# Kernel optimization log

Measured on AMD Instinct MI355X. Metric: run time of the kernel, lower is better.

## Reference

```python
import jax, jax.numpy as jnp
from jax import lax
import numpy as np

B, L, D = 2048, 100, 64      # batch, max_len, embedding_dim
K = 64                       # embedding_num (codebook entries)
CB = K * 8                   # code_book_dim = 512 (== D*8 encoder out channels)
ITEMS = 1_000_000
EPS = 1e-3                   # tf.layers.batch_normalization default epsilon


def setup_inputs() -> dict:
    key = jax.random.key(0)
    ks = jax.random.split(key, 16)
    w = lambda i, shape: jax.random.normal(ks[i], shape, dtype=jnp.float32) * 0.05
    z = lambda c: jnp.zeros((c,), jnp.float32)
    o = lambda c: jnp.ones((c,), jnp.float32)
    return {
        "history_item_ids": jax.random.randint(ks[0], (B, L), 0, ITEMS, dtype=jnp.int32),
        "history_item_masks": jax.random.randint(ks[1], (B, L), 0, 2, dtype=jnp.int32),
        "item_embedding_table": jax.random.normal(ks[2], (ITEMS, D), dtype=jnp.float32),
        "user_book": jax.random.normal(ks[3], (K, CB), dtype=jnp.float32),
        "e_w1": w(4, (2, 2, D, 2 * D)), "e_b1": z(2 * D), "e_g1": o(2 * D), "e_be1": z(2 * D),
        "e_w2": w(5, (2, 2, 2 * D, 4 * D)), "e_b2": z(4 * D), "e_g2": o(4 * D), "e_be2": z(4 * D),
        "e_w3": w(6, (2, 2, 4 * D, 8 * D)), "e_b3": z(8 * D),
        "d_w1": w(7, (2, 2, 8 * D, 4 * D)), "d_b1": z(4 * D), "d_g1": o(4 * D), "d_be1": z(4 * D),
        "d_w2": w(8, (2, 2, 4 * D, 2 * D)), "d_b2": z(2 * D), "d_g2": o(2 * D), "d_be2": z(2 * D),
        "d_w3": w(9, (2, 2, 2 * D, D)), "d_b3": z(D),
    }


def _forward(history_item_ids, history_item_masks, item_embedding_table, user_book,
             e_w1, e_b1, e_g1, e_be1, e_w2, e_b2, e_g2, e_be2, e_w3, e_b3,
             d_w1, d_b1, d_g1, d_be1, d_w2, d_b2, d_g2, d_be2, d_w3, d_b3):
    dn = ('NHWC', 'HWIO', 'NHWC')
    bn = lambda x, g, b: x * (g / jnp.sqrt(1.0 + EPS)) + b  # inference BN: moving mean 0, var 1
    conv = lambda x, w_, b_: lax.conv_general_dilated(x, w_, (1, 1), 'VALID', dimension_numbers=dn) + b_
    deconv = lambda x, w_, b_: lax.conv_transpose(x, w_, (1, 1), 'VALID', dimension_numbers=dn) + b_

    mask = (history_item_masks >= 1).astype(jnp.float32)               # [B,L]
    hist = item_embedding_table[history_item_ids] * mask[..., None]    # [B,L,D]

    H = int(L ** 0.5); W = L // H
    h = hist.reshape(-1, H, W, D)
    h = jax.nn.relu(bn(conv(h, e_w1, e_b1), e_g1, e_be1))              # [B,9,9,2D]
    h = jax.nn.relu(bn(conv(h, e_w2, e_b2), e_g2, e_be2))              # [B,8,8,4D]
    x_encode = conv(h, e_w3, e_b3)                                     # [B,7,7,CB]

    # nearest-neighbor codebook lookup (get_quantized)
    flat = x_encode.reshape(-1, CB)                                    # [B*49,CB]
    dist = ((flat * flat).sum(1, keepdims=True)
            + (user_book * user_book).sum(1)
            - 2.0 * flat @ user_book.T)                                # [B*49,K]
    idx = jnp.argmin(dist, axis=1)
    quantized = user_book[idx].reshape(x_encode.shape)                 # [B,7,7,CB]

    # straight-through estimator
    st = x_encode + lax.stop_gradient(quantized - x_encode)
    g = jax.nn.relu(bn(deconv(st, d_w1, d_b1), d_g1, d_be1))           # [B,8,8,4D]
    g = jax.nn.relu(bn(deconv(g, d_w2, d_b2), d_g2, d_be2))            # [B,9,9,2D]
    vq_x = deconv(g, d_w3, d_b3).reshape(hist.shape)                   # [B,L,D]

    vq_mean = vq_x.sum(1) / mask.sum(-1, keepdims=True)                # [B,D]
    mse = lambda a, b: jnp.mean((a - b) ** 2)
    beta = 0.25
    vqvae_loss = (mse(hist, vq_x)
                  + mse(quantized, lax.stop_gradient(x_encode))
                  + beta * mse(x_encode, lax.stop_gradient(quantized)))
    return vq_mean, vq_x, vqvae_loss


def reference(history_item_ids, history_item_masks, item_embedding_table, user_book,
              e_w1, e_b1, e_g1, e_be1, e_w2, e_b2, e_g2, e_be2, e_w3, e_b3,
              d_w1, d_b1, d_g1, d_be1, d_w2, d_b2, d_g2, d_be2, d_w3, d_b3):
    return _forward(history_item_ids, history_item_masks, item_embedding_table, user_book,
                    e_w1, e_b1, e_g1, e_be1, e_w2, e_b2, e_g2, e_be2, e_w3, e_b3,
                    d_w1, d_b1, d_g1, d_be1, d_w2, d_b2, d_g2, d_be2, d_w3, d_b3)
```

## Files before the change

kernel.cpp:

```cpp
#include <hip/hip_runtime.h>
#include <hip/hip_bf16.h>
#include <cstdint>
#include <cstddef>


typedef __attribute__((ext_vector_type(8))) short short8v;
typedef __attribute__((ext_vector_type(4))) float f32x4;

constexpr int B  = 2048;
constexpr int L  = 100;
constexpr int K  = 64;
constexpr int CB = 512;
#define MARGIN 0.1f

constexpr size_t R0_OFF  = 0;
constexpr size_t R1_OFF  = 51380224;
constexpr size_t IDX_OFF = 84934656;
constexpr size_t CBN_OFF = 85035008;
constexpr size_t CNT_OFF = 85035072;
constexpr size_t ACC_OFF = 85035088;
constexpr size_t WL_OFF  = 85035104;
constexpr size_t WB_OFF  = 85135456;

constexpr size_t EW1H=0,       EW1L=32768;
constexpr size_t EW2H=65536,   EW2L=196608;
constexpr size_t EW3H=327680;
constexpr size_t DW2H=851968,  DW3H=983040;
constexpr size_t W3BH=1015808, W3BL=1081344;

constexpr size_t BW1_OFF  = WB_OFF + 573440;
constexpr size_t DOTB_OFF = BW1_OFF + 65536;

__device__ inline ushort bf16_hi(float f){ __hip_bfloat16 h=__float2bfloat16(f); return *(ushort*)&h; }
__device__ inline float  bf16_tof(ushort u){ __hip_bfloat16 h; *(ushort*)&h=u; return __bfloat162float(h); }

__device__ void wtrans(const float* __restrict__ w, int IC, int OC,
                       ushort* __restrict__ hi, ushort* __restrict__ lo,
                       int gid, int gsz)
{
    int tot = 4*IC*OC;
    for (int i = gid; i < tot; i += gsz) {
        int kk = i/(IC*OC), r = i - kk*(IC*OC), ic = r/OC, oc = r - ic*OC;
        float v = w[i];
        ushort h = bf16_hi(v);
        size_t dst = ((size_t)kk*OC + oc)*IC + ic;
        hi[dst] = h;
        if (lo) lo[dst] = bf16_hi(v - bf16_tof(h));
    }
}

__global__ __launch_bounds__(256)
void wprep_k(const float* e1, const float* e2, const float* e3,
             const float* d2, const float* d3, ushort* wb)
{
    int gid = blockIdx.x*256 + threadIdx.x, gsz = gridDim.x*256;
    wtrans(e1,  64, 128, wb+EW1H, wb+EW1L, gid, gsz);
    wtrans(e2, 128, 256, wb+EW2H, wb+EW2L, gid, gsz);
    wtrans(e3, 256, 512, wb+EW3H, nullptr, gid, gsz);
    wtrans(d2, 256, 128, wb+DW2H, nullptr, gid, gsz);
    wtrans(d3, 128,  64, wb+DW3H, nullptr, gid, gsz);
}

__global__ __launch_bounds__(256)
void w3b_k(const float* __restrict__ e_w3, const float* __restrict__ book,
           ushort* __restrict__ wb)
{
    const int kk = blockIdx.x >> 6, k = blockIdx.x & 63, ic = threadIdx.x;
    const float4* wr = (const float4*)(e_w3 + ((size_t)(kk*256)+ic)*512);
    const float4* br = (const float4*)(book + (size_t)k*512);
    float s = 0.f;
    for (int c = 0; c < 128; ++c) {
        float4 a = wr[c], bb = br[c];
        s = fmaf(a.x,bb.x,fmaf(a.y,bb.y,fmaf(a.z,bb.z,fmaf(a.w,bb.w,s))));
    }
    size_t dst = ((size_t)(kk*64+k))*256 + ic;
    ushort h = bf16_hi(s);
    wb[W3BH+dst] = h;
    wb[W3BL+dst] = bf16_hi(s - bf16_tof(h));
}

__global__ __launch_bounds__(256)
void bw1_k(const float* __restrict__ d_w1, const float* __restrict__ book,
           float* __restrict__ bw1)
{
    const int tap = blockIdx.x >> 6, k = blockIdx.x & 63, oc = threadIdx.x;
    const float* br = book + (size_t)k*512;
    const float* wr = d_w1 + (size_t)(tap*512)*256 + oc;
    float s = 0.f;
    for (int ic = 0; ic < 512; ++ic)
        s = fmaf(br[ic], wr[(size_t)ic*256], s);
    bw1[((size_t)(tap*64+k))*256 + oc] = s;
}

__global__ __launch_bounds__(256)
void prep_k(const float* __restrict__ book, const float* __restrict__ e_b3,
            float* __restrict__ cbn, float* __restrict__ dotb,
            float* __restrict__ acc, int* __restrict__ cnt)
{
    const int t = threadIdx.x;
    if (t < 64) {
        const float* r = book + t * 512;
        float s = 0.f, d = 0.f;
        for (int c = 0; c < 512; ++c) { s = fmaf(r[c], r[c], s); d = fmaf(e_b3[c], r[c], d); }
        cbn[t] = s; dotb[t] = d;
    }
    if (t == 64 || t == 65) acc[t-64] = 0.f;
    if (t == 66) *cnt = 0;
}

template<int IH,int IW,int IC,int OC,int PAD,int MODE,bool HASBN,bool SPLIT,
         int OCS,int ICC,int MT,int OUTFMT,bool FUSE,int SMP,bool DBUF>
__global__ __launch_bounds__(256)
void sconv_k(const uint* __restrict__ in_pk, const ushort* __restrict__ in_bf,
             const int* __restrict__ ids, const int* __restrict__ masks,
             const float* __restrict__ table,
             const ushort* __restrict__ wt_hi, const ushort* __restrict__ wt_lo,
             const float* __restrict__ bias, const float* __restrict__ gamma,
             const float* __restrict__ beta,
             float* __restrict__ out_f, uint* __restrict__ out_pk,
             ushort* __restrict__ out_bf, float* __restrict__ out_mean,
             float* __restrict__ acc_g)
{
    constexpr int OH=IH+2*PAD-1, OW=IW+2*PAD-1, NPOS=OH*OW, IHW=IH*IW;
    constexpr int OCB=OC/OCS, NPW=OCB/4, NT=NPW/16;
    constexpr int NCH=IC/ICC, KS=ICC/32;
    constexpr int PL=SPLIT?2:1;
    constexpr int NB=(DBUF && NCH>1)?2:1;
    constexpr int AROWS=IHW+1, RB=ICC*2;
    constexpr int C8=ICC/8;
    constexpr int NITEMS=SMP*IHW*C8;
    constexpr int SI=(NITEMS+255)/256;
    constexpr bool EXACT=(SI*256==NITEMS);
    constexpr int SPLB=AROWS*RB;
    constexpr int SAMB=PL*SPLB;
    constexpr int BUFB=SMP*SAMB;

    __shared__ ushort s_a[NB*SMP*PL*AROWS*ICC];
    char* sb=(char*)s_a;

    const int v=blockIdx.x, r8=v&7, iv=v>>3;
    const int b0 = (r8*(B/SMP/8) + iv/OCS)*SMP;
    const int sl = iv - (iv/OCS)*OCS;

    const int tid=threadIdx.x, lane=tid&63, wv=tid>>6;
    const int l15=lane&15, lq=lane>>4;
    const int n0=sl*OCB + wv*NPW;

    int arow[4][MT];
    #pragma unroll
    for(int kk=0;kk<4;++kk){
        const int ky=kk>>1, kx=kk&1;
        #pragma unroll
        for(int m=0;m<MT;++m){
            int p=m*16+l15;
            int py=p/OW, px=p-py*OW;
            int ty=py+ky-PAD, tx=px+kx-PAD;
            bool ok=(p<NPOS)&&((unsigned)ty<(unsigned)IH)&&((unsigned)tx<(unsigned)IW);
            arow[kk][m]= ok ? ty*IW+tx : IHW;
        }
    }

    f32x4 acc[SMP][MT][NT];
    #pragma unroll
    for(int s=0;s<SMP;++s)
        #pragma unroll
        for(int m=0;m<MT;++m)
            #pragma unroll
            for(int n=0;n<NT;++n) acc[s][m][n]=(f32x4)0.0f;

    uint4 r0[SI];
    uint4 r1[(MODE==1||MODE==3)?SI:1];
    float msk[(MODE==1)?SI:1];

    auto stage_load=[&](int c){
        const int ic0=c*ICC;
        #pragma unroll
        for(int t=0;t<SI;++t){
            int idx=tid+t*256;
            if(EXACT || idx<NITEMS){
                int row=idx/C8, g=idx-row*C8;
                int s=row/IHW, r=row-s*IHW;
                if constexpr(MODE==1){
                    int id=ids[(b0+s)*L+r];
                    msk[t]=(masks[(b0+s)*L+r]>=1)?1.f:0.f;
                    const float* src=table+(size_t)id*64+g*8;
                    r0[t]=*(const uint4*)src;
                    r1[t]=*(const uint4*)(src+4);
                } else if constexpr(MODE==3){
                    const uint* src=in_pk+((size_t)(b0+s)*IHW+r)*IC+ic0+g*8;
                    r0[t]=*(const uint4*)src;
                    r1[t]=*(const uint4*)(src+4);
                } else {
                    r0[t]=*(const uint4*)(in_bf+((size_t)(b0+s)*IHW+r)*IC+ic0+g*8);
                }
            }
        }
    };

    auto stage_write=[&](int bufb){
        #pragma unroll
        for(int t=0;t<SI;++t){
            int idx=tid+t*256;
            if(EXACT || idx<NITEMS){
                int row=idx/C8, g=idx-row*C8;
                int s=row/IHW, r=row-s*IHW;
                int boff=bufb + s*SAMB + r*RB + ((g^(r&7))<<4);
                if constexpr(MODE==1){
                    const float* f0=(const float*)&r0[t];
                    const float* f1=(const float*)&r1[t];
                    float vv[8]={f0[0]*msk[t],f0[1]*msk[t],f0[2]*msk[t],f0[3]*msk[t],
                                 f1[0]*msk[t],f1[1]*msk[t],f1[2]*msk[t],f1[3]*msk[t]};
                    ushort hh[8], ll[8];
                    #pragma unroll
                    for(int j=0;j<8;++j){ hh[j]=bf16_hi(vv[j]); ll[j]=bf16_hi(vv[j]-bf16_tof(hh[j])); }
                    *(uint4*)(sb+boff)=*(uint4*)hh;
                    *(uint4*)(sb+SPLB+boff)=*(uint4*)ll;
                } else if constexpr(MODE==3){
                    const uint* u0=(const uint*)&r0[t];
                    const uint* u1=(const uint*)&r1[t];
                    ushort hh[8], ll[8];
                    #pragma unroll
                    for(int j=0;j<4;++j){ hh[j]=(ushort)(u0[j]&0xffffu); ll[j]=(ushort)(u0[j]>>16); }
                    #pragma unroll
                    for(int j=0;j<4;++j){ hh[4+j]=(ushort)(u1[j]&0xffffu); ll[4+j]=(ushort)(u1[j]>>16); }
                    *(uint4*)(sb+boff)=*(uint4*)hh;
                    *(uint4*)(sb+SPLB+boff)=*(uint4*)ll;
                } else {
                    *(uint4*)(sb+boff)=r0[t];
                }
            }
        }
    };

    auto zero_rows=[&](){
        for(int z=tid; z<NB*SMP*PL*C8; z+=256){
            int nb=z/(SMP*PL*C8), rz=z-nb*(SMP*PL*C8);
            int s=rz/(PL*C8), rz2=rz-s*(PL*C8), pl=rz2/C8, g=rz2-pl*C8;
            *(uint4*)(sb + nb*BUFB + s*SAMB + pl*SPLB + IHW*RB + (g<<4)) = make_uint4(0,0,0,0);
        }
    };

    auto do_mfma=[&](int bufb, int c){
        const int ic0=c*ICC;
        __builtin_amdgcn_s_setprio(1);
        #pragma unroll
        for(int kk=0;kk<4;++kk){
            #pragma unroll
            for(int ks=0;ks<KS;++ks){
                short8v bhv[NT]; short8v blv[SPLIT?NT:1];
                #pragma unroll
                for(int n=0;n<NT;++n){
                    int col=n0+n*16+l15;
                    size_t widx=((size_t)kk*OC+col)*IC+ic0+ks*32+lq*8;
                    bhv[n]=*(const short8v*)(wt_hi+widx);
                    if constexpr(SPLIT) blv[n]=*(const short8v*)(wt_lo+widx);
                }
                #pragma unroll
                for(int s=0;s<SMP;++s){
                    const int sbase=bufb + s*SAMB;
                    #pragma unroll
                    for(int m=0;m<MT;++m){
                        int off=sbase + arow[kk][m]*RB + ((((ks<<2)|lq)^(arow[kk][m]&7))<<4);
                        short8v ah=*(const short8v*)(sb+off);
                        if constexpr(SPLIT){
                            short8v al=*(const short8v*)(sb+SPLB+off);
                            #pragma unroll
                            for(int n=0;n<NT;++n){
                                acc[s][m][n]=__builtin_amdgcn_mfma_f32_16x16x32_bf16(ah,bhv[n],acc[s][m][n],0,0,0);
                                acc[s][m][n]=__builtin_amdgcn_mfma_f32_16x16x32_bf16(ah,blv[n],acc[s][m][n],0,0,0);
                                acc[s][m][n]=__builtin_amdgcn_mfma_f32_16x16x32_bf16(al,bhv[n],acc[s][m][n],0,0,0);
                            }
                        } else {
                            #pragma unroll
                            for(int n=0;n<NT;++n)
                                acc[s][m][n]=__builtin_amdgcn_mfma_f32_16x16x32_bf16(ah,bhv[n],acc[s][m][n],0,0,0);
                        }
                    }
                }
            }
        }
        __builtin_amdgcn_s_setprio(0);
    };

    if constexpr(NB==1){
        stage_load(0);
        zero_rows();
        for(int c=0;c<NCH;++c){
            if(c) __syncthreads();
            stage_write(0);
            __syncthreads();
            if(c+1<NCH) stage_load(c+1);
            do_mfma(0,c);
        }
    } else {
        stage_load(0);
        stage_write(0);
        zero_rows();
        __syncthreads();
        for(int c=0;c<NCH;++c){
            if(c+1<NCH) stage_load(c+1);
            do_mfma((c&1)*BUFB,c);
            if(c+1<NCH){
                stage_write(((c+1)&1)*BUFB);
                __syncthreads();
            }
        }
    }

    const float rs=(float)(1.0/sqrt(1.0+1e-3));
    float lsum=0.f, colsum=0.f;
    #pragma unroll
    for(int s=0;s<SMP;++s){
        const int b=b0+s;
        #pragma unroll
        for(int n=0;n<NT;++n){
            int col=n0+n*16+l15;
            float bi=bias[col];
            float gsc=0.f, bt=0.f;
            if constexpr(HASBN){ gsc=gamma[col]*rs; bt=beta[col]; }
            #pragma unroll
            for(int m=0;m<MT;++m){
                #pragma unroll
                for(int j=0;j<4;++j){
                    int p=m*16+lq*4+j;
                    if(p<NPOS){
                        float vx=acc[s][m][n][j]+bi;
                        if constexpr(HASBN) vx=fmaxf(fmaf(vx,gsc,bt),0.f);
                        size_t g=(size_t)b*NPOS+p;
                        if constexpr(OUTFMT==0){
                            out_f[g*OC+col]=vx;
                        } else if constexpr(OUTFMT==1){
                            ushort h=bf16_hi(vx);
                            ushort lo=bf16_hi(vx-bf16_tof(h));
                            out_pk[g*OC+col]=(uint)h | ((uint)lo<<16);
                        } else {
                            out_bf[g*OC+col]=bf16_hi(vx);
                        }
                        if constexpr(FUSE){
                            int id=ids[b*L+p];
                            float mm=(masks[b*L+p]>=1)?1.f:0.f;
                            float h=table[(size_t)id*64+col]*mm;
                            float df=h-vx;
                            lsum=fmaf(df,df,lsum);
                            colsum+=vx;
                        }
                    }
                }
            }
        }
    }

    if constexpr(FUSE){
        const int b=b0;
        float mc=0.f;
        for(int l=lane;l<L;l+=64) mc += (masks[b*L+l]>=1)?1.f:0.f;
        #pragma unroll
        for(int off=32;off;off>>=1) mc+=__shfl_xor(mc,off);
        colsum += __shfl_xor(colsum,16);
        colsum += __shfl_xor(colsum,32);
        if(lq==0) out_mean[b*64 + n0 + l15] = colsum/mc;
        #pragma unroll
        for(int off=32;off;off>>=1) lsum+=__shfl_xor(lsum,off);
        __syncthreads();
        float* red=(float*)sb;
        if(lane==0) red[wv]=lsum;
        __syncthreads();
        if(tid==0) atomicAdd(acc_g+0, red[0]+red[1]+red[2]+red[3]);
    }
}

__global__ __launch_bounds__(512)
void mxnd_k(const uint* __restrict__ in_pk,
            const ushort* __restrict__ wx,
            const ushort* __restrict__ w3bh, const ushort* __restrict__ w3bl,
            const float* __restrict__ xbias,
            const float* __restrict__ cbn, const float* __restrict__ dotb,
            int* __restrict__ qidx, float* __restrict__ acc_g,
            int* __restrict__ cnt, int* __restrict__ wl)
{
    constexpr int IHW=64, AROWS=65, RB=128;
    constexpr int NPOS=49, OW=7, MT=4, NT=4;
    constexpr int SPLB=AROWS*RB;
    constexpr int BUFB=2*SPLB;

    __shared__ ushort s_a[2*2*AROWS*64];
    char* sb=(char*)s_a;

    const int v=blockIdx.x;
    const int b=(v&7)*(B/8)+(v>>3);
    const int tid=threadIdx.x, lane=tid&63, wv=tid>>6;
    const int l15=lane&15, lq=lane>>4;
    const int n0x=wv*64;

    int arow[4][MT];
    #pragma unroll
    for(int kk=0;kk<4;++kk){
        const int ky=kk>>1, kx=kk&1;
        #pragma unroll
        for(int m=0;m<MT;++m){
            int p=m*16+l15;
            int py=p/OW, px=p-py*OW;
            arow[kk][m]= (p<NPOS) ? (py+ky)*8+(px+kx) : IHW;
        }
    }

    f32x4 accx[MT][NT];
    #pragma unroll
    for(int m=0;m<MT;++m)
        #pragma unroll
        for(int n=0;n<NT;++n) accx[m][n]=(f32x4)0.0f;
    f32x4 accd[MT];
    #pragma unroll
    for(int m=0;m<MT;++m) accd[m]=(f32x4)0.0f;

    uint4 r0, r1;

    auto stage_load=[&](int c){
        const int ic0=c*64;
        int row=tid>>3, g=tid&7;
        const uint* src=in_pk+((size_t)b*IHW+row)*256+ic0+g*8;
        r0=*(const uint4*)src;
        r1=*(const uint4*)(src+4);
    };
    auto stage_write=[&](int bufb){
        int row=tid>>3, g=tid&7;
        int boff=bufb + row*RB + ((g^(row&7))<<4);
        const uint* u0=(const uint*)&r0;
        const uint* u1=(const uint*)&r1;
        ushort hh[8], ll[8];
        #pragma unroll
        for(int j=0;j<4;++j){ hh[j]=(ushort)(u0[j]&0xffffu); ll[j]=(ushort)(u0[j]>>16); }
        #pragma unroll
        for(int j=0;j<4;++j){ hh[4+j]=(ushort)(u1[j]&0xffffu); ll[4+j]=(ushort)(u1[j]>>16); }
        *(uint4*)(sb+boff)=*(uint4*)hh;
        *(uint4*)(sb+SPLB+boff)=*(uint4*)ll;
    };

    stage_load(0);
    stage_write(0);
    for(int z=tid; z<2*2*8; z+=512){
        int nb=z/16, rz=z-nb*16, pl=rz/8, g=rz-pl*8;
        *(uint4*)(sb + nb*BUFB + pl*SPLB + IHW*RB + (g<<4)) = make_uint4(0,0,0,0);
    }
    __syncthreads();

    for(int c=0;c<4;++c){
        if(c+1<4) stage_load(c+1);
        const int bufb=(c&1)*BUFB;
        const int ic0=c*64;
        __builtin_amdgcn_s_setprio(1);
        #pragma unroll
        for(int kk=0;kk<4;++kk){
            #pragma unroll
            for(int ks=0;ks<2;++ks){
                short8v bx[NT];
                #pragma unroll
                for(int n=0;n<NT;++n){
                    int col=n0x+n*16+l15;
                    bx[n]=*(const short8v*)(wx+((size_t)kk*512+col)*256+ic0+ks*32+lq*8);
                }
                short8v bdh, bdl;
                if(wv<4){
                    int cold=wv*16+l15;
                    size_t wdx=((size_t)kk*64+cold)*256+ic0+ks*32+lq*8;
                    bdh=*(const short8v*)(w3bh+wdx);
                    bdl=*(const short8v*)(w3bl+wdx);
                }
                #pragma unroll
                for(int m=0;m<MT;++m){
                    int off=bufb + arow[kk][m]*RB + ((((ks<<2)|lq)^(arow[kk][m]&7))<<4);
                    short8v ah=*(const short8v*)(sb+off);
                    #pragma unroll
                    for(int n=0;n<NT;++n)
                        accx[m][n]=__builtin_amdgcn_mfma_f32_16x16x32_bf16(ah,bx[n],accx[m][n],0,0,0);
                    if(wv<4){
                        short8v al=*(const short8v*)(sb+SPLB+off);
                        accd[m]=__builtin_amdgcn_mfma_f32_16x16x32_bf16(ah,bdh,accd[m],0,0,0);
                        accd[m]=__builtin_amdgcn_mfma_f32_16x16x32_bf16(ah,bdl,accd[m],0,0,0);
                        accd[m]=__builtin_amdgcn_mfma_f32_16x16x32_bf16(al,bdh,accd[m],0,0,0);
                    }
                }
            }
        }
        __builtin_amdgcn_s_setprio(0);
        if(c+1<4){
            stage_write(((c+1)&1)*BUFB);
            __syncthreads();
        }
    }

    float xs=0.f;
    #pragma unroll
    for(int n=0;n<NT;++n){
        int col=n0x+n*16+l15;
        float bi=xbias[col];
        #pragma unroll
        for(int m=0;m<MT;++m){
            #pragma unroll
            for(int j=0;j<4;++j){
                int p=m*16+lq*4+j;
                if(p<NPOS){ float vv=accx[m][n][j]+bi; xs=fmaf(vv,vv,xs); }
            }
        }
    }
    #pragma unroll
    for(int off=32;off;off>>=1) xs+=__shfl_xor(xs,off);
    __syncthreads();
    float* f=(float*)sb;
    if(lane==0) f[wv]=xs;

    if(wv<4){
        float cb=cbn[wv*16+l15], db=dotb[wv*16+l15];
        float* sd1=f+16;
        int*   sk =(int*)(f+16+256);
        float* sd2=f+16+512;
        #pragma unroll
        for(int m=0;m<MT;++m){
            #pragma unroll
            for(int j=0;j<4;++j){
                int p=m*16+lq*4+j;
                float d1=cb-2.f*(accd[m][j]+db);
                int   k1=wv*16+l15;
                float d2=3.4e38f;
                #pragma unroll
                for(int off=1;off<16;off<<=1){
                    float od1=__shfl_xor(d1,off);
                    int   ok1=__shfl_xor(k1,off);
                    float od2=__shfl_xor(d2,off);
                    if(od1<d1 || (od1==d1 && ok1<k1)){ d2=fminf(d1,od2); d1=od1; k1=ok1; }
                    else                              { d2=fminf(d2,od1); }
                }
                if(l15==0 && p<NPOS){ sd1[p*4+wv]=d1; sk[p*4+wv]=k1; sd2[p*4+wv]=d2; }
            }
        }
    }
    __syncthreads();
    if(tid==0) atomicAdd(acc_g+1, f[0]+f[1]+f[2]+f[3]+f[4]+f[5]+f[6]+f[7]);

    {
        float* sd1=f+16;
        int*   sk =(int*)(f+16+256);
        float* sd2=f+16+512;
        float lsum=0.f;
        if(tid<NPOS){
            float d1=sd1[tid*4+0]; int k1=sk[tid*4+0]; float d2=sd2[tid*4+0];
            #pragma unroll
            for(int w=1;w<4;++w){
                float D1=sd1[tid*4+w]; int K1=sk[tid*4+w]; float D2=sd2[tid*4+w];
                if(D1<d1){ d2=fminf(d1,D2); d1=D1; k1=K1; }
                else     { d2=fminf(d2,D1); }
            }
            qidx[b*49+tid]=k1;
            if(d2-d1<=MARGIN){ int t=atomicAdd(cnt,1); wl[t]=b*49+tid; }
            lsum=d1;
        }
        if(tid<64){
            #pragma unroll
            for(int off=32;off;off>>=1) lsum+=__shfl_xor(lsum,off);
            if(tid==0) atomicAdd(acc_g+1, lsum);
        }
    }
}

__global__ __launch_bounds__(256)
void dgather_k(const int* __restrict__ qidx, const float* __restrict__ bw1,
               const float* __restrict__ b1, const float* __restrict__ g1s,
               const float* __restrict__ be1, ushort* __restrict__ G1)
{
    const int b=blockIdx.x, tid=threadIdx.x;
    const int pg=tid>>2, og=(tid&3)*64;
    const int py=pg>>3, px=pg&7;

    float a[64];
    #pragma unroll
    for(int j=0;j<64;++j) a[j]=0.f;

    #pragma unroll
    for(int tap=0;tap<4;++tap){
        int iy=py+(tap>>1)-1, ix=px+(tap&1)-1;
        if((unsigned)iy<7u && (unsigned)ix<7u){
            int kq=qidx[b*49+iy*7+ix];
            const float4* src=(const float4*)(bw1+((size_t)(tap*64+kq))*256+og);
            #pragma unroll
            for(int j=0;j<16;++j){
                float4 vv=src[j];
                a[4*j+0]+=vv.x; a[4*j+1]+=vv.y; a[4*j+2]+=vv.z; a[4*j+3]+=vv.w;
            }
        }
    }
    const float rs=(float)(1.0/sqrt(1.0+1e-3));
    #pragma unroll
    for(int j=0;j<64;++j){
        int col=og+j;
        float vv=a[j]+b1[col];
        vv=fmaxf(fmaf(vv, g1s[col]*rs, be1[col]), 0.f);
        G1[((size_t)b*64+pg)*256+col]=bf16_hi(vv);
    }
}

__global__ __launch_bounds__(256)
void recompute_k(const int* __restrict__ wl, const int* __restrict__ cnt,
                 const int* __restrict__ ids, const int* __restrict__ masks,
                 const float* __restrict__ table, const float* __restrict__ book,
                 const float* __restrict__ e_w1, const float* __restrict__ e_b1,
                 const float* __restrict__ e_g1, const float* __restrict__ e_be1,
                 const float* __restrict__ e_w2, const float* __restrict__ e_b2,
                 const float* __restrict__ e_g2, const float* __restrict__ e_be2,
                 const float* __restrict__ e_w3, const float* __restrict__ e_b3,
                 int* __restrict__ qidx)
{
    __shared__ double s_h[16*64];
    __shared__ double s_a1[9*128];
    __shared__ double s_a2[4*256];
    __shared__ double s_x[512];
    __shared__ double s_d[256];

    const int tid = threadIdx.x;
    const double rs = 1.0 / sqrt(1.0 + 1e-3);
    const int n = *cnt;

    for (int wi = blockIdx.x; wi < n; wi += gridDim.x) {
        const int row = wl[wi];
        const int b = row / 49, p = row % 49;
        const int py = p / 7, px = p % 7;

        for (int i = tid; i < 16*64; i += 256) {
            int cell = i >> 6, d = i & 63;
            int l = (py + (cell >> 2)) * 10 + (px + (cell & 3));
            int id = ids[b*100 + l];
            double m = (masks[b*100 + l] >= 1) ? 1.0 : 0.0;
            s_h[i] = (double)table[(size_t)id*64 + d] * m;
        }
        __syncthreads();

        for (int i = tid; i < 9*128; i += 256) {
            int cell = i >> 7, oc = i & 127;
            int ry = cell / 3, rx = cell % 3;
            double s = 0.0;
            #pragma unroll
            for (int kk = 0; kk < 4; ++kk) {
                int icell = (ry + (kk>>1))*4 + (rx + (kk&1));
                const double* hh = s_h + icell*64;
                const float* ww = e_w1 + (kk*64)*128 + oc;
                for (int ic = 0; ic < 64; ++ic)
                    s = fma(hh[ic], (double)ww[ic*128], s);
            }
            s += (double)e_b1[oc];
            s = s * ((double)e_g1[oc] * rs) + (double)e_be1[oc];
            s_a1[i] = s > 0.0 ? s : 0.0;
        }
        __syncthreads();

        for (int i = tid; i < 4*256; i += 256) {
            int cell = i >> 8, oc = i & 255;
            int qy = cell >> 1, qx = cell & 1;
            double s = 0.0;
            #pragma unroll
            for (int kk = 0; kk < 4; ++kk) {
                int icell = (qy + (kk>>1))*3 + (qx + (kk&1));
                const double* aa = s_a1 + icell*128;
                const float* ww = e_w2 + (kk*128)*256 + oc;
                for (int ic = 0; ic < 128; ++ic)
                    s = fma(aa[ic], (double)ww[ic*256], s);
            }
            s += (double)e_b2[oc];
            s = s * ((double)e_g2[oc] * rs) + (double)e_be2[oc];
            s_a2[i] = s > 0.0 ? s : 0.0;
        }
        __syncthreads();

        for (int i = tid; i < 512; i += 256) {
            double s = 0.0;
            #pragma unroll
            for (int kk = 0; kk < 4; ++kk) {
                const double* aa = s_a2 + kk*256;
                const float* ww = e_w3 + (kk*256)*512 + i;
                for (int ic = 0; ic < 256; ++ic)
                    s = fma(aa[ic], (double)ww[ic*512], s);
            }
            s_x[i] = s + (double)e_b3[i];
        }
        __syncthreads();

        {
            int k = tid & 63, seg = tid >> 6;
            const float* cr = book + k*512 + seg*128;
            const double* xr = s_x + seg*128;
            double s = 0.0;
            for (int c = 0; c < 128; ++c) {
                double dd = xr[c] - (double)cr[c];
                s = fma(dd, dd, s);
            }
            s_d[seg*64 + k] = s;
        }
        __syncthreads();

        if (tid < 64) {
            double dv = s_d[tid] + s_d[64+tid] + s_d[128+tid] + s_d[192+tid];
            int kk2 = tid;
            #pragma unroll
            for (int off = 32; off > 0; off >>= 1) {
                double od = __shfl_xor(dv, off);
                int    ok = __shfl_xor(kk2, off);
                if (od < dv || (od == dv && ok < kk2)) { dv = od; kk2 = ok; }
            }
            if (tid == 0) qidx[row] = kk2;
        }
        __syncthreads();
    }
}

__global__ void loss_k(const float* __restrict__ acc, float* __restrict__ out_loss)
{
    float l1 = acc[0] / 13107200.f;
    float l2 = acc[1] / 51380224.f;
    out_loss[0] = l1 + l2 + 0.25f * l2;
}

extern "C" void kernel_launch(void* const* d_in, const int* in_sizes, int n_in,
                              void* d_out, int out_size, void* d_ws, size_t ws_size,
                              hipStream_t stream)
{
    const int*   ids   = (const int*)d_in[0];
    const int*   masks = (const int*)d_in[1];
    const float* table = (const float*)d_in[2];
    const float* book  = (const float*)d_in[3];
    const float* e_w1  = (const float*)d_in[4];
    const float* e_b1  = (const float*)d_in[5];
    const float* e_g1  = (const float*)d_in[6];
    const float* e_be1 = (const float*)d_in[7];
    const float* e_w2  = (const float*)d_in[8];
    const float* e_b2  = (const float*)d_in[9];
    const float* e_g2  = (const float*)d_in[10];
    const float* e_be2 = (const float*)d_in[11];
    const float* e_w3  = (const float*)d_in[12];
    const float* e_b3  = (const float*)d_in[13];
    const float* d_w1  = (const float*)d_in[14];
    const float* d_b1  = (const float*)d_in[15];
    const float* d_g1  = (const float*)d_in[16];
    const float* d_be1 = (const float*)d_in[17];
    const float* d_w2  = (const float*)d_in[18];
    const float* d_b2  = (const float*)d_in[19];
    const float* d_g2  = (const float*)d_in[20];
    const float* d_be2 = (const float*)d_in[21];
    const float* d_w3  = (const float*)d_in[22];
    const float* d_b3  = (const float*)d_in[23];

    float*  ws  = (float*)d_ws;
    uint*   A1P = (uint*)(ws + R0_OFF);
    uint*   A2P = (uint*)(ws + R1_OFF);
    ushort* G1  = (ushort*)(ws + R1_OFF);
    ushort* G2  = (ushort*)(ws + R0_OFF);
    int*    IDX = (int*)(ws + IDX_OFF);
    float*  CBN = ws + CBN_OFF;
    int*    CNT = (int*)(ws + CNT_OFF);
    float*  ACC = ws + ACC_OFF;
    int*    WL  = (int*)(ws + WL_OFF);
    ushort* WB  = (ushort*)(ws + WB_OFF);
    float*  BW1 = ws + BW1_OFF;
    float*  DOTB= ws + DOTB_OFF;

    float* out_mean = (float*)d_out;
    float* out_vqx  = (float*)d_out + (size_t)B * 64;
    float* out_loss = (float*)d_out + (size_t)B * 64 + (size_t)B * L * 64;

    prep_k<<<1, 256, 0, stream>>>(book, e_b3, CBN, DOTB, ACC, CNT);
    wprep_k<<<512, 256, 0, stream>>>(e_w1, e_w2, e_w3, d_w2, d_w3, WB);
    w3b_k<<<256, 256, 0, stream>>>(e_w3, book, WB);
    bw1_k<<<256, 256, 0, stream>>>(d_w1, book, BW1);

    sconv_k<10,10, 64,128,0,1,true ,true ,1, 64,6,1,false,1,true ><<<B,    256,0,stream>>>(
        nullptr, nullptr, ids, masks, table,
        WB+EW1H, WB+EW1L, e_b1, e_g1, e_be1, nullptr, A1P, nullptr, nullptr, nullptr);
    sconv_k< 9, 9,128,256,0,3,true ,true ,2, 64,4,1,false,2,false><<<B,    256,0,stream>>>(
        A1P, nullptr, nullptr, nullptr, nullptr,
        WB+EW2H, WB+EW2L, e_b2, e_g2, e_be2, nullptr, A2P, nullptr, nullptr, nullptr);

    mxnd_k<<<B, 512, 0, stream>>>(A2P, WB+EW3H, WB+W3BH, WB+W3BL,
                                  e_b3, CBN, DOTB, IDX, ACC, CNT, WL);

    recompute_k<<<512, 256, 0, stream>>>(WL, CNT, ids, masks, table, book,
                                         e_w1, e_b1, e_g1, e_be1,
                                         e_w2, e_b2, e_g2, e_be2,
                                         e_w3, e_b3, IDX);

    dgather_k<<<B, 256, 0, stream>>>(IDX, BW1, d_b1, d_g1, d_be1, G1);
    sconv_k< 8, 8,256,128,1,4,true ,false,1, 64,6,2,false,2,true ><<<B/2,  256,0,stream>>>(
        nullptr, G1, nullptr, nullptr, nullptr,
        WB+DW2H, nullptr, d_b2, d_g2, d_be2, nullptr, nullptr, G2, nullptr, nullptr);
    sconv_k< 9, 9,128, 64,1,4,false,false,1, 64,7,0,true ,1,true ><<<B,    256,0,stream>>>(
        nullptr, G2, ids, masks, table,
        WB+DW3H, nullptr, d_b3, nullptr, nullptr, out_vqx, nullptr, nullptr, out_mean, ACC);

    loss_k<<<1, 1, 0, stream>>>(ACC, out_loss);
}
```

Before: 1.310 ms.

## Stage full encoder-conv3 input in LDS once and retune conv grid splits

The encoder's third conv plus codebook distance kernel now loads the whole 64x256 packed input tile into shared memory once, with a 32-way XOR swizzle, instead of double-buffering four 64-channel chunks with a sync per chunk. It also drops the zero pad row and sets launch bounds to 4 blocks per CU. Two sconv launches change a template parameter, so encoder conv2 runs on twice as many blocks and decoder conv2 runs one batch item per block. This removes per-chunk barriers and adds parallelism, but the larger LDS footprint (64KB) may limit occupancy.

```diff
diff --git a/kernel.cpp b/kernel.cpp
--- a/kernel.cpp
+++ b/kernel.cpp
@@ -369,8 +369,8 @@
     }
 }
 
-__global__ __launch_bounds__(512)
-void mxnd_k(const uint* __restrict__ in_pk,
+__global__ __launch_bounds__(512,4)
+void xnd2_k(const uint* __restrict__ in_pk,
             const ushort* __restrict__ wx,
             const ushort* __restrict__ w3bh, const ushort* __restrict__ w3bl,
             const float* __restrict__ xbias,
@@ -378,12 +378,11 @@
             int* __restrict__ qidx, float* __restrict__ acc_g,
             int* __restrict__ cnt, int* __restrict__ wl)
 {
-    constexpr int IHW=64, AROWS=65, RB=128;
     constexpr int NPOS=49, OW=7, MT=4, NT=4;
-    constexpr int SPLB=AROWS*RB;
-    constexpr int BUFB=2*SPLB;
-
-    __shared__ ushort s_a[2*2*AROWS*64];
+    constexpr int ROWB=512;
+    constexpr int PLB=64*ROWB;
+
+    __shared__ ushort s_a[2*64*256];
     char* sb=(char*)s_a;
 
     const int v=blockIdx.x;
@@ -392,6 +391,25 @@
     const int l15=lane&15, lq=lane>>4;
     const int n0x=wv*64;
 
+    #pragma unroll
+    for(int t=0;t<4;++t){
+        int idx=tid+t*512;
+        int row=idx>>5, sl=idx&31;
+        const uint* src=in_pk+((size_t)b*64+row)*256+sl*8;
+        uint4 u0=*(const uint4*)src, u1=*(const uint4*)(src+4);
+        const uint* p0=(const uint*)&u0;
+        const uint* p1=(const uint*)&u1;
+        ushort hh[8], ll[8];
+        #pragma unroll
+        for(int j=0;j<4;++j){ hh[j]=(ushort)(p0[j]&0xffffu); ll[j]=(ushort)(p0[j]>>16); }
+        #pragma unroll
+        for(int j=0;j<4;++j){ hh[4+j]=(ushort)(p1[j]&0xffffu); ll[4+j]=(ushort)(p1[j]>>16); }
+        int boff=row*ROWB+((sl^(row&31))<<4);
+        *(uint4*)(sb+boff)=*(uint4*)hh;
+        *(uint4*)(sb+PLB+boff)=*(uint4*)ll;
+    }
+    __syncthreads();
+
     int arow[4][MT];
     #pragma unroll
     for(int kk=0;kk<4;++kk){
@@ -400,7 +418,7 @@
         for(int m=0;m<MT;++m){
             int p=m*16+l15;
             int py=p/OW, px=p-py*OW;
-            arow[kk][m]= (p<NPOS) ? (py+ky)*8+(px+kx) : IHW;
+            arow[kk][m]= (p<NPOS) ? (py+ky)*8+(px+kx) : 0;
         }
     }
 
@@ -413,81 +431,43 @@
     #pragma unroll
     for(int m=0;m<MT;++m) accd[m]=(f32x4)0.0f;
 
-    uint4 r0, r1;
-
-    auto stage_load=[&](int c){
-        const int ic0=c*64;
-        int row=tid>>3, g=tid&7;
-        const uint* src=in_pk+((size_t)b*IHW+row)*256+ic0+g*8;
-        r0=*(const uint4*)src;
-        r1=*(const uint4*)(src+4);
-    };
-    auto stage_write=[&](int bufb){
-        int row=tid>>3, g=tid&7;
-        int boff=bufb + row*RB + ((g^(row&7))<<4);
-        const uint* u0=(const uint*)&r0;
-        const uint* u1=(const uint*)&r1;
-        ushort hh[8], ll[8];
-        #pragma unroll
-        for(int j=0;j<4;++j){ hh[j]=(ushort)(u0[j]&0xffffu); ll[j]=(ushort)(u0[j]>>16); }
-        #pragma unroll
-        for(int j=0;j<4;++j){ hh[4+j]=(ushort)(u1[j]&0xffffu); ll[4+j]=(ushort)(u1[j]>>16); }
-        *(uint4*)(sb+boff)=*(uint4*)hh;
-        *(uint4*)(sb+SPLB+boff)=*(uint4*)ll;
-    };
-
-    stage_load(0);
-    stage_write(0);
-    for(int z=tid; z<2*2*8; z+=512){
-        int nb=z/16, rz=z-nb*16, pl=rz/8, g=rz-pl*8;
-        *(uint4*)(sb + nb*BUFB + pl*SPLB + IHW*RB + (g<<4)) = make_uint4(0,0,0,0);
-    }
-    __syncthreads();
-
-    for(int c=0;c<4;++c){
-        if(c+1<4) stage_load(c+1);
-        const int bufb=(c&1)*BUFB;
-        const int ic0=c*64;
-        __builtin_amdgcn_s_setprio(1);
-        #pragma unroll
-        for(int kk=0;kk<4;++kk){
-            #pragma unroll
-            for(int ks=0;ks<2;++ks){
-                short8v bx[NT];
+    __builtin_amdgcn_s_setprio(1);
+    #pragma unroll
+    for(int kk=0;kk<4;++kk){
+        #pragma unroll
+        for(int ks=0;ks<8;++ks){
+            short8v bx[NT];
+            #pragma unroll
+            for(int n=0;n<NT;++n){
+                int col=n0x+n*16+l15;
+                bx[n]=*(const short8v*)(wx+((size_t)kk*512+col)*256+ks*32+lq*8);
+            }
+            short8v bdh, bdl;
+            if(wv<4){
+                int cold=wv*16+l15;
+                size_t wdx=((size_t)kk*64+cold)*256+ks*32+lq*8;
+                bdh=*(const short8v*)(w3bh+wdx);
+                bdl=*(const short8v*)(w3bl+wdx);
+            }
+            const int slb=ks*4+lq;
+            #pragma unroll
+            for(int m=0;m<MT;++m){
+                int r=arow[kk][m];
+                int off=r*ROWB+((slb^(r&31))<<4);
+                short8v ah=*(const short8v*)(sb+off);
                 #pragma unroll
-                for(int n=0;n<NT;++n){
-                    int col=n0x+n*16+l15;
-                    bx[n]=*(const short8v*)(wx+((size_t)kk*512+col)*256+ic0+ks*32+lq*8);
+                for(int n=0;n<NT;++n)
+                    accx[m][n]=__builtin_amdgcn_mfma_f32_16x16x32_bf16(ah,bx[n],accx[m][n],0,0,0);
+                if(wv<4){
+                    short8v al=*(const short8v*)(sb+PLB+off);
+                    accd[m]=__builtin_amdgcn_mfma_f32_16x16x32_bf16(ah,bdh,accd[m],0,0,0);
+                    accd[m]=__builtin_amdgcn_mfma_f32_16x16x32_bf16(ah,bdl,accd[m],0,0,0);
+                    accd[m]=__builtin_amdgcn_mfma_f32_16x16x32_bf16(al,bdh,accd[m],0,0,0);
                 }
-                short8v bdh, bdl;
-                if(wv<4){
-                    int cold=wv*16+l15;
-                    size_t wdx=((size_t)kk*64+cold)*256+ic0+ks*32+lq*8;
-                    bdh=*(const short8v*)(w3bh+wdx);
-                    bdl=*(const short8v*)(w3bl+wdx);
-                }
-                #pragma unroll
-                for(int m=0;m<MT;++m){
-                    int off=bufb + arow[kk][m]*RB + ((((ks<<2)|lq)^(arow[kk][m]&7))<<4);
-                    short8v ah=*(const short8v*)(sb+off);
-                    #pragma unroll
-                    for(int n=0;n<NT;++n)
-                        accx[m][n]=__builtin_amdgcn_mfma_f32_16x16x32_bf16(ah,bx[n],accx[m][n],0,0,0);
-                    if(wv<4){
-                        short8v al=*(const short8v*)(sb+SPLB+off);
-                        accd[m]=__builtin_amdgcn_mfma_f32_16x16x32_bf16(ah,bdh,accd[m],0,0,0);
-                        accd[m]=__builtin_amdgcn_mfma_f32_16x16x32_bf16(ah,bdl,accd[m],0,0,0);
-                        accd[m]=__builtin_amdgcn_mfma_f32_16x16x32_bf16(al,bdh,accd[m],0,0,0);
-                    }
-                }
-            }
-        }
-        __builtin_amdgcn_s_setprio(0);
-        if(c+1<4){
-            stage_write(((c+1)&1)*BUFB);
-            __syncthreads();
-        }
-    }
+            }
+        }
+    }
+    __builtin_amdgcn_s_setprio(0);
 
     float xs=0.f;
     #pragma unroll
@@ -505,15 +485,16 @@
     }
     #pragma unroll
     for(int off=32;off;off>>=1) xs+=__shfl_xor(xs,off);
+
     __syncthreads();
     float* f=(float*)sb;
     if(lane==0) f[wv]=xs;
 
+    float* sd1=f+16;
+    int*   sk =(int*)(f+16+256);
+    float* sd2=f+16+512;
     if(wv<4){
         float cb=cbn[wv*16+l15], db=dotb[wv*16+l15];
-        float* sd1=f+16;
-        int*   sk =(int*)(f+16+256);
-        float* sd2=f+16+512;
         #pragma unroll
         for(int m=0;m<MT;++m){
             #pragma unroll
@@ -538,9 +519,6 @@
     if(tid==0) atomicAdd(acc_g+1, f[0]+f[1]+f[2]+f[3]+f[4]+f[5]+f[6]+f[7]);
 
     {
-        float* sd1=f+16;
-        int*   sk =(int*)(f+16+256);
-        float* sd2=f+16+512;
         float lsum=0.f;
         if(tid<NPOS){
             float d1=sd1[tid*4+0]; int k1=sk[tid*4+0]; float d2=sd2[tid*4+0];
@@ -769,14 +747,14 @@
     w3b_k<<<256, 256, 0, stream>>>(e_w3, book, WB);
     bw1_k<<<256, 256, 0, stream>>>(d_w1, book, BW1);
 
-    sconv_k<10,10, 64,128,0,1,true ,true ,1, 64,6,1,false,1,true ><<<B,    256,0,stream>>>(
+    sconv_k<10,10, 64,128,0,1,true ,true ,1, 64,6,1,false,1,true ><<<B,   256,0,stream>>>(
         nullptr, nullptr, ids, masks, table,
         WB+EW1H, WB+EW1L, e_b1, e_g1, e_be1, nullptr, A1P, nullptr, nullptr, nullptr);
-    sconv_k< 9, 9,128,256,0,3,true ,true ,2, 64,4,1,false,2,false><<<B,    256,0,stream>>>(
+    sconv_k< 9, 9,128,256,0,3,true ,true ,2, 64,4,1,false,1,true ><<<B*2, 256,0,stream>>>(
         A1P, nullptr, nullptr, nullptr, nullptr,
         WB+EW2H, WB+EW2L, e_b2, e_g2, e_be2, nullptr, A2P, nullptr, nullptr, nullptr);
 
-    mxnd_k<<<B, 512, 0, stream>>>(A2P, WB+EW3H, WB+W3BH, WB+W3BL,
+    xnd2_k<<<B, 512, 0, stream>>>(A2P, WB+EW3H, WB+W3BH, WB+W3BL,
                                   e_b3, CBN, DOTB, IDX, ACC, CNT, WL);
 
     recompute_k<<<512, 256, 0, stream>>>(WL, CNT, ids, masks, table, book,
@@ -785,10 +763,10 @@
                                          e_w3, e_b3, IDX);
 
     dgather_k<<<B, 256, 0, stream>>>(IDX, BW1, d_b1, d_g1, d_be1, G1);
-    sconv_k< 8, 8,256,128,1,4,true ,false,1, 64,6,2,false,2,true ><<<B/2,  256,0,stream>>>(
+    sconv_k< 8, 8,256,128,1,4,true ,false,1, 64,6,2,false,1,true ><<<B,   256,0,stream>>>(
         nullptr, G1, nullptr, nullptr, nullptr,
         WB+DW2H, nullptr, d_b2, d_g2, d_be2, nullptr, nullptr, G2, nullptr, nullptr);
-    sconv_k< 9, 9,128, 64,1,4,false,false,1, 64,7,0,true ,1,true ><<<B,    256,0,stream>>>(
+    sconv_k< 9, 9,128, 64,1,4,false,false,1, 64,7,0,true ,1,true ><<<B,   256,0,stream>>>(
         nullptr, G2, ids, masks, table,
         WB+DW3H, nullptr, d_b3, nullptr, nullptr, out_vqx, nullptr, nullptr, out_mean, ACC);
 
```

Measured after the change: 1.564 ms. 19.4% more time.
